# Optimization experiments

Measured on AMD Instinct MI355X. Metric: run time of the kernel, lower is better.

The kernel has to match this reference:

```python
import jax, jax.numpy as jnp
import numpy as np

B, L, D_IN = 2048, 512, 32
PRED_LEN = 96
COND = 128      # cond_dim (z_dim)
XPROJ = 128     # x_proj_dim defaults to cond_dim
ODE_H = 128     # ode_hidden
TDIM = 128      # time_dim
HID = 256       # hidden of final MLP
N_STEPS = 32    # fixed-step RK4 steps over t in [0,1] (stands in for adaptive dopri5)
LN_EPS = 1e-5


def _linear(x, w, b):
    return x @ w.T + b


def _layernorm(x, g, b):
    mu = jnp.mean(x, axis=-1, keepdims=True)
    var = jnp.var(x, axis=-1, keepdims=True)
    return (x - mu) * jax.lax.rsqrt(var + LN_EPS) * g + b


def _interp(x_seq, t):
    # linear interp over sequence dim: x_seq (B,L,D), scalar t in [0,1] -> (B,D)
    Ls = x_seq.shape[1]
    pos = jnp.clip(t, 0.0, 1.0) * (Ls - 1)
    i0 = jnp.clip(jnp.floor(pos).astype(jnp.int32), 0, Ls - 1)
    i1 = jnp.clip(i0 + 1, 0, Ls - 1)
    w = (pos - i0.astype(pos.dtype))
    x0 = jax.lax.dynamic_index_in_dim(x_seq, i0, axis=1, keepdims=False)
    x1 = jax.lax.dynamic_index_in_dim(x_seq, i1, axis=1, keepdims=False)
    return (1.0 - w) * x0 + w * x1


def setup_inputs() -> dict:
    key = jax.random.key(0)
    ks = jax.random.split(key, 16)

    def kaiming(k, shape):
        return jax.random.normal(k, shape, jnp.float32) * np.float32(np.sqrt(2.0 / shape[-1]))

    IN_F = PRED_LEN * D_IN + COND + TDIM   # 3328
    OUT_F = PRED_LEN * D_IN                # 3072
    return {
        "x_t": jax.random.normal(ks[0], (B, PRED_LEN, D_IN), jnp.float32),
        "past": jax.random.normal(ks[1], (B, L, D_IN), jnp.float32),
        "t": jax.random.randint(ks[2], (B,), 0, 1000),
        "xproj_w": kaiming(ks[3], (XPROJ, D_IN)), "xproj_b": jnp.zeros((XPROJ,), jnp.float32),
        "z0_w": kaiming(ks[4], (COND, XPROJ)), "z0_b": jnp.zeros((COND,), jnp.float32),
        "ln_g": jnp.ones((COND,), jnp.float32), "ln_b": jnp.zeros((COND,), jnp.float32),
        "w1": kaiming(ks[5], (ODE_H, COND + XPROJ)), "b1": jnp.zeros((ODE_H,), jnp.float32),
        "w2": kaiming(ks[6], (ODE_H, ODE_H)), "b2": jnp.zeros((ODE_H,), jnp.float32),
        "w3": kaiming(ks[7], (COND, ODE_H)), "b3": jnp.zeros((COND,), jnp.float32),
        "fw1": kaiming(ks[8], (HID, IN_F)), "fb1": jnp.zeros((HID,), jnp.float32),
        "fw2": kaiming(ks[9], (HID, HID)), "fb2": jnp.zeros((HID,), jnp.float32),
        "fw3": kaiming(ks[10], (OUT_F, HID)), "fb3": jnp.zeros((OUT_F,), jnp.float32),
    }


def _time_emb(t):
    half = TDIM // 2
    freqs = jnp.exp(-np.float32(np.log(10000.0)) * jnp.arange(half, dtype=jnp.float32) / (half - 1))
    args = t.astype(jnp.float32)[:, None] * freqs[None, :]
    return jnp.concatenate([jnp.sin(args), jnp.cos(args)], axis=1)  # (B, TDIM)


def _forward(x_t, past, t, xproj_w, xproj_b, z0_w, z0_b, ln_g, ln_b,
             w1, b1, w2, b2, w3, b3, fw1, fb1, fw2, fb2, fw3, fb3):
    Bn = x_t.shape[0]
    x_seq = _linear(past, xproj_w, xproj_b)           # (B,L,XPROJ)
    z0 = _linear(x_seq[:, 0, :], z0_w, z0_b)          # (B,COND)

    def odef(tt, z):
        xt = _interp(x_seq, tt)                       # (B,XPROJ)
        zn = _layernorm(z, ln_g, ln_b)
        h = jnp.concatenate([zn, xt], axis=-1)
        h = jax.nn.silu(_linear(h, w1, b1))
        h = jax.nn.silu(_linear(h, w2, b2))
        return _linear(h, w3, b3)                     # (B,COND)

    dt = jnp.float32(1.0 / N_STEPS)

    def step(z, tt):
        k1 = odef(tt, z)
        k2 = odef(tt + dt * 0.5, z + dt * 0.5 * k1)
        k3 = odef(tt + dt * 0.5, z + dt * 0.5 * k2)
        k4 = odef(tt + dt, z + dt * k3)
        return z + (dt / 6.0) * (k1 + 2.0 * k2 + 2.0 * k3 + k4), None

    ts = jnp.arange(N_STEPS, dtype=jnp.float32) * dt
    cond, _ = jax.lax.scan(step, z0, ts)              # zT (B,COND)

    temb = _time_emb(t)                               # (B,TDIM)
    x_flat = x_t.reshape(Bn, -1)                      # (B,PRED_LEN*D_IN)
    h = jnp.concatenate([x_flat, cond, temb], axis=1)
    h = jax.nn.silu(_linear(h, fw1, fb1))
    h = jax.nn.silu(_linear(h, fw2, fb2))
    eps = _linear(h, fw3, fb3)
    return eps.reshape(Bn, PRED_LEN, D_IN)


def reference(x_t, past, t, xproj_w, xproj_b, z0_w, z0_b, ln_g, ln_b,
              w1, b1, w2, b2, w3, b3, fw1, fb1, fw2, fb2, fw3, fb3):
    return _forward(x_t, past, t, xproj_w, xproj_b, z0_w, z0_b, ln_g, ln_b,
                    w1, b1, w2, b2, w3, b3, fw1, fb1, fw2, fb2, fw3, fb3)
```

## Files before the change

### kernel.cpp

```cpp
#include <hip/hip_runtime.h>
#include <math.h>

typedef _Float16 h8f16 __attribute__((ext_vector_type(8)));
typedef _Float16 h2f16 __attribute__((ext_vector_type(2)));
typedef float f32x4 __attribute__((ext_vector_type(4)));

#define MFMA16(a, b, c) __builtin_amdgcn_mfma_f32_16x16x32_f16((a), (b), (c), 0, 0, 0)

__device__ __forceinline__ float silu_f(float v) {
    return v * __builtin_amdgcn_rcpf(1.0f + __expf(-v));
}

__device__ __forceinline__ void bar_lds() {
    asm volatile("s_waitcnt lgkmcnt(0)" ::: "memory");
    __builtin_amdgcn_s_barrier();
    __builtin_amdgcn_sched_barrier(0);
}

__global__ __launch_bounds__(512, 1) void ode_kernel(
    const float* __restrict__ past,
    const float* __restrict__ xproj_w, const float* __restrict__ xproj_b,
    const float* __restrict__ z0_w, const float* __restrict__ z0_b,
    const float* __restrict__ ln_g, const float* __restrict__ ln_b,
    const float* __restrict__ w1, const float* __restrict__ b1,
    const float* __restrict__ w2, const float* __restrict__ b2,
    const float* __restrict__ w3, const float* __restrict__ b3,
    float* __restrict__ zbuf)
{
    __shared__ _Float16 hbuf[16][136];
    __shared__ _Float16 h1S[16][136];
    __shared__ _Float16 h2S[16][136];
    __shared__ float    pS[16][33];
    __shared__ float    x0S[16][128];
    __shared__ float    zS0[16][129];

    const int tid  = threadIdx.x;
    const int wid  = tid >> 6;
    const int lane = tid & 63;
    const int lrow = lane & 15;
    const int lhi  = lane >> 4;
    const int b0   = blockIdx.x * 16;
    const int nc   = wid * 16 + lrow;
    const int koff = lhi * 8;

    h8f16 w1f[4], wcf, w2f[4], w3f[4];
    float b1t, b2r, b3r;
    {
#pragma unroll
        for (int ks = 0; ks < 4; ++ks) {
            h8f16 v1, v2, v3;
#pragma unroll
            for (int j = 0; j < 8; ++j) {
                const int k = ks * 32 + koff + j;
                v1[j] = (_Float16)(w1[nc * 256 + k] * ln_g[k]);
                v2[j] = (_Float16)w2[nc * 128 + k];
                v3[j] = (_Float16)w3[nc * 128 + k];
            }
            w1f[ks] = v1; w2f[ks] = v2; w3f[ks] = v3;
        }
        float wc[8] = {0, 0, 0, 0, 0, 0, 0, 0};
        float bc = 0.0f, bb = 0.0f;
        const float* w1a = w1 + nc * 256;
        const float* w1b = w1a + 128;
#pragma unroll 4
        for (int k = 0; k < 128; ++k) {
            const float a = w1b[k];
            bc += a * xproj_b[k];
            bb += w1a[k] * ln_b[k];
            const float* xr = xproj_w + k * 32 + koff;
#pragma unroll
            for (int j = 0; j < 8; ++j) wc[j] += a * xr[j];
        }
        h8f16 v;
#pragma unroll
        for (int j = 0; j < 8; ++j) v[j] = (_Float16)wc[j];
        wcf = v;
        b1t = b1[nc] + bc + bb;
        b2r = b2[nc]; b3r = b3[nc];
    }

    pS[tid >> 5][tid & 31] = past[(long)(b0 + (tid >> 5)) * 16384 + (tid & 31)];
    __syncthreads();
    {
        const int r  = tid >> 5;
        const int c0 = (tid & 31) * 4;
#pragma unroll
        for (int cc = 0; cc < 4; ++cc) {
            const int kc = c0 + cc;
            float s = xproj_b[kc];
            const float* xr = xproj_w + kc * 32;
#pragma unroll
            for (int c = 0; c < 32; ++c) s += pS[r][c] * xr[c];
            x0S[r][kc] = s;
        }
    }
    __syncthreads();
    {
        const int nn = tid & 127;
        const int r0 = (tid >> 7) * 4;
        for (int p = 0; p < 4; ++p) {
            const int r = r0 + p;
            float s = z0_b[nn];
            const float* zr = z0_w + nn * 128;
            for (int k = 0; k < 128; ++k) s += x0S[r][k] * zr[k];
            zS0[r][nn] = s;
        }
    }
    __syncthreads();

    float zc[4], krk[4];
#pragma unroll
    for (int j = 0; j < 4; ++j) {
        zc[j] = zS0[4 * lhi + j][nc];
        hbuf[4 * lhi + j][nc] = (_Float16)zc[j];
    }

    const float DT = 1.0f / 32.0f;

    f32x4 s0a, s0b, s1a, s1b;
    auto stage = [&](int e) {
        const float pos = (float)e * 7.984375f;
        const int i0 = (int)pos;
        const int i1 = (i0 < 511) ? i0 + 1 : 511;
        const float* base = past + (long)(b0 + lrow) * 16384;
        const float* p0 = base + i0 * 32 + koff;
        const float* p1 = base + i1 * 32 + koff;
        s0a = *(const f32x4*)p0; s0b = *(const f32x4*)(p0 + 4);
        s1a = *(const f32x4*)p1; s1b = *(const f32x4*)(p1 + 4);
    };
    auto blend = [&](int e) -> h8f16 {
        const float pos = (float)e * 7.984375f;
        const float w = pos - floorf(pos);
        h8f16 r;
#pragma unroll
        for (int j = 0; j < 4; ++j) {
            r[j]     = (_Float16)(s0a[j] + w * (s1a[j] - s0a[j]));
            r[4 + j] = (_Float16)(s0b[j] + w * (s1b[j] - s0b[j]));
        }
        return r;
    };

    const h2f16 one2 = {(_Float16)1.0f, (_Float16)1.0f};

    auto phaseA = [&](h8f16 bxc) {
        h8f16 xf[4];
#pragma unroll
        for (int ks = 0; ks < 4; ++ks)
            xf[ks] = *(const h8f16*)&hbuf[lrow][ks * 32 + koff];
        float s0 = 0.f, s1 = 0.f, q0 = 0.f, q1 = 0.f;
#pragma unroll
        for (int ks = 0; ks < 4; ++ks) {
#pragma unroll
            for (int p = 0; p < 4; ++p) {
                const h2f16 x2 = {xf[ks][2 * p], xf[ks][2 * p + 1]};
                if (p & 1) {
                    s1 = __builtin_amdgcn_fdot2(x2, one2, s1, false);
                    q1 = __builtin_amdgcn_fdot2(x2, x2, q1, false);
                } else {
                    s0 = __builtin_amdgcn_fdot2(x2, one2, s0, false);
                    q0 = __builtin_amdgcn_fdot2(x2, x2, q0, false);
                }
            }
        }
        float s = s0 + s1, q = q0 + q1;
        s += __shfl_xor(s, 16); q += __shfl_xor(q, 16);
        s += __shfl_xor(s, 32); q += __shfl_xor(q, 32);
        const float mu  = s * (1.0f / 128.0f);
        const float var = q * (1.0f / 128.0f) - mu * mu;
        const float inv = 1.0f / sqrtf(var + 1e-5f);
        const _Float16 ih = (_Float16)inv;
        const _Float16 mh = (_Float16)(-mu * inv);
        h8f16 ip, mp;
#pragma unroll
        for (int j = 0; j < 8; ++j) { ip[j] = ih; mp[j] = mh; }
        f32x4 acc = {0, 0, 0, 0};
#pragma unroll
        for (int ks = 0; ks < 4; ++ks) {
            const h8f16 az = xf[ks] * ip + mp;
            acc = MFMA16(az, w1f[ks], acc);
        }
        acc = MFMA16(bxc, wcf, acc);
#pragma unroll
        for (int j = 0; j < 4; ++j)
            h1S[4 * lhi + j][nc] = (_Float16)silu_f(acc[j] + b1t);
    };
    auto phaseB = [&]() {
        f32x4 acc = {0, 0, 0, 0};
#pragma unroll
        for (int ks = 0; ks < 4; ++ks) {
            const h8f16 a = *(const h8f16*)&h1S[lrow][ks * 32 + koff];
            acc = MFMA16(a, w2f[ks], acc);
        }
#pragma unroll
        for (int j = 0; j < 4; ++j)
            h2S[4 * lhi + j][nc] = (_Float16)silu_f(acc[j] + b2r);
    };
    auto phaseC = [&]() -> f32x4 {
        f32x4 acc = {0, 0, 0, 0};
#pragma unroll
        for (int ks = 0; ks < 4; ++ks) {
            const h8f16 a = *(const h8f16*)&h2S[lrow][ks * 32 + koff];
            acc = MFMA16(a, w3f[ks], acc);
        }
#pragma unroll
        for (int j = 0; j < 4; ++j) acc[j] += b3r;
        return acc;
    };

    stage(0);
    h8f16 bxc = blend(0);
    __syncthreads();

#pragma unroll 1
    for (int st = 0; st < 32; ++st) {
        const int e1 = 2 * st + 1, e2 = 2 * st + 2;
        phaseA(bxc);
        stage(e1);
        bar_lds();
        phaseB(); bar_lds();
        {
            const f32x4 k = phaseC();
#pragma unroll
            for (int j = 0; j < 4; ++j) {
                krk[j] = k[j];
                hbuf[4 * lhi + j][nc] = (_Float16)(zc[j] + 0.5f * DT * k[j]);
            }
        }
        bar_lds();
        bxc = blend(e1);
        phaseA(bxc); bar_lds();
        phaseB(); bar_lds();
        {
            const f32x4 k = phaseC();
#pragma unroll
            for (int j = 0; j < 4; ++j) {
                krk[j] += 2.0f * k[j];
                hbuf[4 * lhi + j][nc] = (_Float16)(zc[j] + 0.5f * DT * k[j]);
            }
        }
        bar_lds();
        phaseA(bxc);
        stage(e2);
        bar_lds();
        phaseB(); bar_lds();
        {
            const f32x4 k = phaseC();
#pragma unroll
            for (int j = 0; j < 4; ++j) {
                krk[j] += 2.0f * k[j];
                hbuf[4 * lhi + j][nc] = (_Float16)(zc[j] + DT * k[j]);
            }
        }
        bar_lds();
        bxc = blend(e2);
        phaseA(bxc); bar_lds();
        phaseB(); bar_lds();
        {
            const f32x4 k = phaseC();
#pragma unroll
            for (int j = 0; j < 4; ++j) {
                zc[j] += (DT / 6.0f) * (krk[j] + k[j]);
                hbuf[4 * lhi + j][nc] = (_Float16)zc[j];
            }
        }
        bar_lds();
    }

#pragma unroll
    for (int j = 0; j < 4; ++j)
        zbuf[(long)(b0 + 4 * lhi + j) * 128 + nc] = zc[j];
}

__global__ __launch_bounds__(256) void temb_kernel(
    const int* __restrict__ tvals, _Float16* __restrict__ tbuf)
{
    const int tid = threadIdx.x;
#pragma unroll 1
    for (int c = 0; c < 8; ++c) {
        const int chunk = blockIdx.x * 256 + tid + c * 4096;
        const int b  = chunk >> 4;
        const int j0 = (chunk & 15) * 8;
        const float tv = (float)tvals[b];
        h8f16 v;
#pragma unroll
        for (int j = 0; j < 8; ++j) {
            const int jj  = j0 + j;
            const int idx = (jj < 64) ? jj : jj - 64;
            const float fr = expf(-9.210340371976184f * (float)idx * (1.0f / 63.0f));
            const float a  = tv * fr;
            v[j] = (_Float16)((jj < 64) ? sinf(a) : cosf(a));
        }
        *(h8f16*)&tbuf[(long)b * 128 + j0] = v;
    }
}

__global__ __launch_bounds__(256) void gemm1d_kernel(
    const float* __restrict__ x_t, const float* __restrict__ cond,
    const _Float16* __restrict__ tbuf,
    const float* __restrict__ fw1, const float* __restrict__ fb1,
    _Float16* __restrict__ h1)
{
    __shared__ _Float16 aS[64][40];
    __shared__ _Float16 wS[64][40];
    const int mb = blockIdx.x * 64, nb = blockIdx.y * 64;
    const int tid = threadIdx.x, lane = tid & 63, wq = tid >> 6;
    const int lrow = lane & 15, lhi = lane >> 4;
    f32x4 acc[4];
#pragma unroll
    for (int nt = 0; nt < 4; ++nt) acc[nt] = (f32x4){0, 0, 0, 0};

    const int sr = tid >> 2;
    const int sk = (tid & 3) * 8;

    for (int k0 = 0; k0 < 3328; k0 += 32) {
        if (k0 < 3072) {
            const float* s = x_t + (long)(mb + sr) * 3072 + k0 + sk;
            const f32x4 u0 = *(const f32x4*)s;
            const f32x4 u1 = *(const f32x4*)(s + 4);
            h8f16 v;
#pragma unroll
            for (int j = 0; j < 4; ++j) { v[j] = (_Float16)u0[j]; v[4 + j] = (_Float16)u1[j]; }
            *(h8f16*)&aS[sr][sk] = v;
        } else if (k0 < 3200) {
            const float* s = cond + (long)(mb + sr) * 128 + (k0 - 3072) + sk;
            const f32x4 u0 = *(const f32x4*)s;
            const f32x4 u1 = *(const f32x4*)(s + 4);
            h8f16 v;
#pragma unroll
            for (int j = 0; j < 4; ++j) { v[j] = (_Float16)u0[j]; v[4 + j] = (_Float16)u1[j]; }
            *(h8f16*)&aS[sr][sk] = v;
        } else {
            *(h8f16*)&aS[sr][sk] =
                *(const h8f16*)&tbuf[(long)(mb + sr) * 128 + (k0 - 3200) + sk];
        }
        {
            const float* s = fw1 + (long)(nb + sr) * 3328 + k0 + sk;
            h8f16 v;
#pragma unroll
            for (int j = 0; j < 8; ++j) v[j] = (_Float16)s[j];
            *(h8f16*)&wS[sr][sk] = v;
        }
        __syncthreads();
        const h8f16 a = *(const h8f16*)&aS[wq * 16 + lrow][lhi * 8];
#pragma unroll
        for (int nt = 0; nt < 4; ++nt) {
            const h8f16 bfr = *(const h8f16*)&wS[nt * 16 + lrow][lhi * 8];
            acc[nt] = MFMA16(a, bfr, acc[nt]);
        }
        __syncthreads();
    }

#pragma unroll
    for (int nt = 0; nt < 4; ++nt) {
        const int cc = nb + nt * 16 + lrow;
        const float bv = fb1[cc];
#pragma unroll
        for (int j = 0; j < 4; ++j) {
            const int rr = mb + wq * 16 + lhi * 4 + j;
            h1[(long)rr * 256 + cc] = (_Float16)silu_f(acc[nt][j] + bv);
        }
    }
}

template <bool SILU, bool OUT_F16>
__global__ __launch_bounds__(256) void gemm_f16(
    const _Float16* __restrict__ A, const float* __restrict__ W,
    const float* __restrict__ bias, void* __restrict__ out,
    int M, int N, int K)
{
    __shared__ _Float16 aS[64][40];
    __shared__ _Float16 wS[64][40];
    const int mb = blockIdx.x * 64, nb = blockIdx.y * 64;
    const int tid = threadIdx.x, lane = tid & 63, wq = tid >> 6;
    const int lrow = lane & 15, lhi = lane >> 4;
    f32x4 acc[4];
#pragma unroll
    for (int nt = 0; nt < 4; ++nt) acc[nt] = (f32x4){0, 0, 0, 0};

    const int sr = tid >> 2;
    const int sk = (tid & 3) * 8;

    for (int k0 = 0; k0 < K; k0 += 32) {
        {
            h8f16 v = *(const h8f16*)&A[(long)(mb + sr) * K + k0 + sk];
            *(h8f16*)&aS[sr][sk] = v;
        }
        {
            const float* s = &W[(long)(nb + sr) * K + k0 + sk];
            h8f16 v;
#pragma unroll
            for (int j = 0; j < 8; ++j) v[j] = (_Float16)s[j];
            *(h8f16*)&wS[sr][sk] = v;
        }
        __syncthreads();
        h8f16 a = *(const h8f16*)&aS[wq * 16 + lrow][lhi * 8];
#pragma unroll
        for (int nt = 0; nt < 4; ++nt) {
            h8f16 bfr = *(const h8f16*)&wS[nt * 16 + lrow][lhi * 8];
            acc[nt] = MFMA16(a, bfr, acc[nt]);
        }
        __syncthreads();
    }

#pragma unroll
    for (int nt = 0; nt < 4; ++nt) {
        const int cc = nb + nt * 16 + lrow;
        const float bv = bias[cc];
#pragma unroll
        for (int j = 0; j < 4; ++j) {
            const int rr = mb + wq * 16 + lhi * 4 + j;
            float v = acc[nt][j] + bv;
            if (SILU) v = silu_f(v);
            if (OUT_F16) ((_Float16*)out)[(long)rr * N + cc] = (_Float16)v;
            else         ((float*)out)[(long)rr * N + cc] = v;
        }
    }
}

extern "C" void kernel_launch(void* const* d_in, const int* in_sizes, int n_in,
                              void* d_out, int out_size, void* d_ws, size_t ws_size,
                              hipStream_t stream)
{
    const float* x_t     = (const float*)d_in[0];
    const float* past    = (const float*)d_in[1];
    const int*   tvals   = (const int*)d_in[2];
    const float* xproj_w = (const float*)d_in[3];
    const float* xproj_b = (const float*)d_in[4];
    const float* z0_w    = (const float*)d_in[5];
    const float* z0_b    = (const float*)d_in[6];
    const float* ln_g    = (const float*)d_in[7];
    const float* ln_b    = (const float*)d_in[8];
    const float* w1      = (const float*)d_in[9];
    const float* b1      = (const float*)d_in[10];
    const float* w2      = (const float*)d_in[11];
    const float* b2      = (const float*)d_in[12];
    const float* w3      = (const float*)d_in[13];
    const float* b3      = (const float*)d_in[14];
    const float* fw1     = (const float*)d_in[15];
    const float* fb1     = (const float*)d_in[16];
    const float* fw2     = (const float*)d_in[17];
    const float* fb2     = (const float*)d_in[18];
    const float* fw3     = (const float*)d_in[19];
    const float* fb3     = (const float*)d_in[20];

    char* ws = (char*)d_ws;
    float*     zbuf = (float*)ws;
    _Float16*  tbuf = (_Float16*)(ws + (1 << 20));
    _Float16*  h1   = (_Float16*)(ws + 2 * (1 << 20));
    _Float16*  h2   = (_Float16*)(ws + 3 * (1 << 20));

    ode_kernel<<<128, 512, 0, stream>>>(past, xproj_w, xproj_b, z0_w, z0_b,
                                        ln_g, ln_b, w1, b1, w2, b2, w3, b3, zbuf);

    temb_kernel<<<16, 256, 0, stream>>>(tvals, tbuf);

    gemm1d_kernel<<<dim3(32, 4), 256, 0, stream>>>(x_t, zbuf, tbuf, fw1, fb1, h1);

    gemm_f16<true,  true ><<<dim3(32, 4),  256, 0, stream>>>(h1, fw2, fb2, h2, 2048, 256, 256);
    gemm_f16<false, false><<<dim3(32, 48), 256, 0, stream>>>(h2, fw3, fb3, d_out, 2048, 3072, 256);
}
```

Before: 362.0 us.

## Overlap fp16 conversion of inputs and weights with ODE blocks in one launch

The ODE kernel grows 104 extra blocks that run alongside the 128 ODE blocks on otherwise idle CUs. They convert x_t and the fw1/fw2/fw3 weights to fp16, compute the time embedding, and write these into a concatenated fp16 activation buffer and fp16 weight copies. The downstream GEMMs then load fp16 directly instead of converting fp32 on every tile, which halves their global traffic and drops the separate temb kernel launch. In exchange the full conversion pass writes extra data to the workspace each call, and the extra blocks may compete with the latency-bound ODE blocks for memory bandwidth.

Measured after the change: 297.8 us. 17.7% less time.

```diff
diff --git a/kernel.cpp b/kernel.cpp
--- a/kernel.cpp
+++ b/kernel.cpp
@@ -17,7 +17,7 @@
     __builtin_amdgcn_sched_barrier(0);
 }
 
-__global__ __launch_bounds__(512, 1) void ode_kernel(
+__global__ __launch_bounds__(512, 1) void fat_kernel(
     const float* __restrict__ past,
     const float* __restrict__ xproj_w, const float* __restrict__ xproj_b,
     const float* __restrict__ z0_w, const float* __restrict__ z0_b,
@@ -25,7 +25,12 @@
     const float* __restrict__ w1, const float* __restrict__ b1,
     const float* __restrict__ w2, const float* __restrict__ b2,
     const float* __restrict__ w3, const float* __restrict__ b3,
-    float* __restrict__ zbuf)
+    const float* __restrict__ x_t, const int* __restrict__ tvals,
+    const float* __restrict__ fw1, const float* __restrict__ fw2,
+    const float* __restrict__ fw3,
+    float* __restrict__ zbuf, _Float16* __restrict__ hcat,
+    _Float16* __restrict__ fw1h, _Float16* __restrict__ fw2h,
+    _Float16* __restrict__ fw3h)
 {
     __shared__ _Float16 hbuf[16][136];
     __shared__ _Float16 h1S[16][136];
@@ -34,7 +39,51 @@
     __shared__ float    x0S[16][128];
     __shared__ float    zS0[16][129];
 
-    const int tid  = threadIdx.x;
+    const int tid = threadIdx.x;
+
+    if (blockIdx.x >= 128) {
+        const int fid = blockIdx.x - 128;
+        for (long c = fid * 512 + tid; c < 1032192; c += 104 * 512) {
+            if (c < 786432) {
+                const long b = c / 384, q = (c % 384) * 8;
+                const float* s = x_t + b * 3072 + q;
+                const f32x4 u0 = *(const f32x4*)s;
+                const f32x4 u1 = *(const f32x4*)(s + 4);
+                h8f16 v;
+#pragma unroll
+                for (int j = 0; j < 4; ++j) { v[j] = (_Float16)u0[j]; v[4 + j] = (_Float16)u1[j]; }
+                *(h8f16*)&hcat[b * 3328 + q] = v;
+            } else if (c < 819200) {
+                const long u = c - 786432;
+                const long b = u >> 4;
+                const int j0 = (int)(u & 15) * 8;
+                const float tv = (float)tvals[b];
+                h8f16 v;
+#pragma unroll
+                for (int j = 0; j < 8; ++j) {
+                    const int jj  = j0 + j;
+                    const int idx = (jj < 64) ? jj : jj - 64;
+                    const float fr = expf(-9.210340371976184f * (float)idx * (1.0f / 63.0f));
+                    const float a  = tv * fr;
+                    v[j] = (_Float16)((jj < 64) ? sinf(a) : cosf(a));
+                }
+                *(h8f16*)&hcat[b * 3328 + 3200 + j0] = v;
+            } else {
+                const float* src; _Float16* dst; long off;
+                if (c < 925696)      { src = fw1; dst = fw1h; off = (c - 819200) * 8; }
+                else if (c < 933888) { src = fw2; dst = fw2h; off = (c - 925696) * 8; }
+                else                 { src = fw3; dst = fw3h; off = (c - 933888) * 8; }
+                const f32x4 u0 = *(const f32x4*)(src + off);
+                const f32x4 u1 = *(const f32x4*)(src + off + 4);
+                h8f16 v;
+#pragma unroll
+                for (int j = 0; j < 4; ++j) { v[j] = (_Float16)u0[j]; v[4 + j] = (_Float16)u1[j]; }
+                *(h8f16*)&dst[off] = v;
+            }
+        }
+        return;
+    }
+
     const int wid  = tid >> 6;
     const int lane = tid & 63;
     const int lrow = lane & 15;
@@ -271,33 +320,9 @@
         zbuf[(long)(b0 + 4 * lhi + j) * 128 + nc] = zc[j];
 }
 
-__global__ __launch_bounds__(256) void temb_kernel(
-    const int* __restrict__ tvals, _Float16* __restrict__ tbuf)
-{
-    const int tid = threadIdx.x;
-#pragma unroll 1
-    for (int c = 0; c < 8; ++c) {
-        const int chunk = blockIdx.x * 256 + tid + c * 4096;
-        const int b  = chunk >> 4;
-        const int j0 = (chunk & 15) * 8;
-        const float tv = (float)tvals[b];
-        h8f16 v;
-#pragma unroll
-        for (int j = 0; j < 8; ++j) {
-            const int jj  = j0 + j;
-            const int idx = (jj < 64) ? jj : jj - 64;
-            const float fr = expf(-9.210340371976184f * (float)idx * (1.0f / 63.0f));
-            const float a  = tv * fr;
-            v[j] = (_Float16)((jj < 64) ? sinf(a) : cosf(a));
-        }
-        *(h8f16*)&tbuf[(long)b * 128 + j0] = v;
-    }
-}
-
-__global__ __launch_bounds__(256) void gemm1d_kernel(
-    const float* __restrict__ x_t, const float* __restrict__ cond,
-    const _Float16* __restrict__ tbuf,
-    const float* __restrict__ fw1, const float* __restrict__ fb1,
+__global__ __launch_bounds__(256) void gemm1z_kernel(
+    const _Float16* __restrict__ hcat, const float* __restrict__ cond,
+    const _Float16* __restrict__ fw1h, const float* __restrict__ fb1,
     _Float16* __restrict__ h1)
 {
     __shared__ _Float16 aS[64][40];
@@ -313,15 +338,7 @@
     const int sk = (tid & 3) * 8;
 
     for (int k0 = 0; k0 < 3328; k0 += 32) {
-        if (k0 < 3072) {
-            const float* s = x_t + (long)(mb + sr) * 3072 + k0 + sk;
-            const f32x4 u0 = *(const f32x4*)s;
-            const f32x4 u1 = *(const f32x4*)(s + 4);
-            h8f16 v;
-#pragma unroll
-            for (int j = 0; j < 4; ++j) { v[j] = (_Float16)u0[j]; v[4 + j] = (_Float16)u1[j]; }
-            *(h8f16*)&aS[sr][sk] = v;
-        } else if (k0 < 3200) {
+        if (k0 >= 3072 && k0 < 3200) {
             const float* s = cond + (long)(mb + sr) * 128 + (k0 - 3072) + sk;
             const f32x4 u0 = *(const f32x4*)s;
             const f32x4 u1 = *(const f32x4*)(s + 4);
@@ -331,15 +348,9 @@
             *(h8f16*)&aS[sr][sk] = v;
         } else {
             *(h8f16*)&aS[sr][sk] =
-                *(const h8f16*)&tbuf[(long)(mb + sr) * 128 + (k0 - 3200) + sk];
-        }
-        {
-            const float* s = fw1 + (long)(nb + sr) * 3328 + k0 + sk;
-            h8f16 v;
-#pragma unroll
-            for (int j = 0; j < 8; ++j) v[j] = (_Float16)s[j];
-            *(h8f16*)&wS[sr][sk] = v;
-        }
+                *(const h8f16*)&hcat[(long)(mb + sr) * 3328 + k0 + sk];
+        }
+        *(h8f16*)&wS[sr][sk] = *(const h8f16*)&fw1h[(long)(nb + sr) * 3328 + k0 + sk];
         __syncthreads();
         const h8f16 a = *(const h8f16*)&aS[wq * 16 + lrow][lhi * 8];
 #pragma unroll
@@ -363,8 +374,8 @@
 }
 
 template <bool SILU, bool OUT_F16>
-__global__ __launch_bounds__(256) void gemm_f16(
-    const _Float16* __restrict__ A, const float* __restrict__ W,
+__global__ __launch_bounds__(256) void gemm_ff(
+    const _Float16* __restrict__ A, const _Float16* __restrict__ W,
     const float* __restrict__ bias, void* __restrict__ out,
     int M, int N, int K)
 {
@@ -381,22 +392,13 @@
     const int sk = (tid & 3) * 8;
 
     for (int k0 = 0; k0 < K; k0 += 32) {
-        {
-            h8f16 v = *(const h8f16*)&A[(long)(mb + sr) * K + k0 + sk];
-            *(h8f16*)&aS[sr][sk] = v;
-        }
-        {
-            const float* s = &W[(long)(nb + sr) * K + k0 + sk];
-            h8f16 v;
-#pragma unroll
-            for (int j = 0; j < 8; ++j) v[j] = (_Float16)s[j];
-            *(h8f16*)&wS[sr][sk] = v;
-        }
+        *(h8f16*)&aS[sr][sk] = *(const h8f16*)&A[(long)(mb + sr) * K + k0 + sk];
+        *(h8f16*)&wS[sr][sk] = *(const h8f16*)&W[(long)(nb + sr) * K + k0 + sk];
         __syncthreads();
-        h8f16 a = *(const h8f16*)&aS[wq * 16 + lrow][lhi * 8];
+        const h8f16 a = *(const h8f16*)&aS[wq * 16 + lrow][lhi * 8];
 #pragma unroll
         for (int nt = 0; nt < 4; ++nt) {
-            h8f16 bfr = *(const h8f16*)&wS[nt * 16 + lrow][lhi * 8];
+            const h8f16 bfr = *(const h8f16*)&wS[nt * 16 + lrow][lhi * 8];
             acc[nt] = MFMA16(a, bfr, acc[nt]);
         }
         __syncthreads();
@@ -445,17 +447,20 @@
 
     char* ws = (char*)d_ws;
     float*     zbuf = (float*)ws;
-    _Float16*  tbuf = (_Float16*)(ws + (1 << 20));
-    _Float16*  h1   = (_Float16*)(ws + 2 * (1 << 20));
-    _Float16*  h2   = (_Float16*)(ws + 3 * (1 << 20));
-
-    ode_kernel<<<128, 512, 0, stream>>>(past, xproj_w, xproj_b, z0_w, z0_b,
-                                        ln_g, ln_b, w1, b1, w2, b2, w3, b3, zbuf);
-
-    temb_kernel<<<16, 256, 0, stream>>>(tvals, tbuf);
-
-    gemm1d_kernel<<<dim3(32, 4), 256, 0, stream>>>(x_t, zbuf, tbuf, fw1, fb1, h1);
-
-    gemm_f16<true,  true ><<<dim3(32, 4),  256, 0, stream>>>(h1, fw2, fb2, h2, 2048, 256, 256);
-    gemm_f16<false, false><<<dim3(32, 48), 256, 0, stream>>>(h2, fw3, fb3, d_out, 2048, 3072, 256);
-}
+    _Float16*  hcat = (_Float16*)(ws + (1 << 20));
+    _Float16*  h1   = (_Float16*)(ws + 15 * (1 << 20));
+    _Float16*  h2   = (_Float16*)(ws + 16 * (1 << 20));
+    _Float16*  fw1h = (_Float16*)(ws + 17 * (1 << 20));
+    _Float16*  fw2h = (_Float16*)(ws + 19 * (1 << 20));
+    _Float16*  fw3h = (_Float16*)(ws + 20 * (1 << 20));
+
+    fat_kernel<<<232, 512, 0, stream>>>(past, xproj_w, xproj_b, z0_w, z0_b,
+                                        ln_g, ln_b, w1, b1, w2, b2, w3, b3,
+                                        x_t, tvals, fw1, fw2, fw3,
+                                        zbuf, hcat, fw1h, fw2h, fw3h);
+
+    gemm1z_kernel<<<dim3(32, 4), 256, 0, stream>>>(hcat, zbuf, fw1h, fb1, h1);
+
+    gemm_ff<true,  true ><<<dim3(32, 4),  256, 0, stream>>>(h1, fw2h, fb2, h2, 2048, 256, 256);
+    gemm_ff<false, false><<<dim3(32, 48), 256, 0, stream>>>(h2, fw3h, fb3, d_out, 2048, 3072, 256);
+}
```
